# Kernel optimization log

Hardware: AMD Instinct MI355X
Metric: run time of the kernel (lower is better)

The kernel has to match this reference:

```python
import jax, jax.numpy as jnp
import numpy as np
import math

B, T, C, H = 2, 2048, 1024, 16
D = C // H  # head dim = 64

def setup_inputs() -> dict:
    key = jax.random.key(0)
    ks = jax.random.split(key, 5)
    scale_in = 1.0 / math.sqrt(C)
    x = jax.random.normal(ks[0], (B, T, C), dtype=jnp.float32)
    W_attn = jax.random.normal(ks[1], (C, 3 * C), dtype=jnp.float32) * scale_in
    b_attn = jnp.zeros((3 * C,), dtype=jnp.float32)
    W_proj = jax.random.normal(ks[2], (C, C), dtype=jnp.float32) * scale_in
    b_proj = jnp.zeros((C,), dtype=jnp.float32)
    return {"x": x, "W_attn": W_attn, "b_attn": b_attn, "W_proj": W_proj, "b_proj": b_proj}

def reference(x, W_attn, b_attn, W_proj, b_proj):
    qkv = x @ W_attn + b_attn                      # [B,T,3C]
    q, k, v = jnp.split(qkv, 3, axis=2)            # each [B,T,C]
    def heads(t):
        return t.reshape(B, T, H, D).transpose(0, 2, 1, 3)  # [B,H,T,D]
    q, k, v = heads(q), heads(k), heads(v)
    # NOTE: original scales by 1/sqrt(n_embd), not 1/sqrt(head_dim)
    scores = jnp.einsum('bhtd,bhsd->bhts', q, k) / math.sqrt(C)  # [B,H,T,T]
    mask = jnp.tril(jnp.ones((T, T), dtype=scores.dtype))
    scores = scores + (mask - 1.0) * 1e9
    attn = jax.nn.softmax(scores, axis=-1)
    out = jnp.einsum('bhts,bhsd->bhtd', attn, v)   # [B,H,T,D]
    out = out.transpose(0, 2, 1, 3).reshape(B, T, C)
    return out @ W_proj + b_proj
```

## Files before the change

kernel.cpp:

```cpp
#include <hip/hip_runtime.h>
#include <hip/hip_bf16.h>


typedef __attribute__((ext_vector_type(8))) short bf16x8;
typedef __attribute__((ext_vector_type(4))) short bf16x4;
typedef __attribute__((ext_vector_type(4))) float f32x4;

__device__ __forceinline__ short f2bs(float f) {
    union { __hip_bfloat16 h; short s; } u;
    u.h = __float2bfloat16(f);
    return u.s;
}

__device__ __forceinline__ short f2bs_trunc(float f) {
    return (short)(__float_as_uint(f) >> 16);
}

#define GLOAD_LDS16(gp, lp)                                                        \
    __builtin_amdgcn_global_load_lds((const __attribute__((address_space(1))) void*)(gp), \
                                     (__attribute__((address_space(3))) void*)(lp), 16, 0, 0)

__global__ __launch_bounds__(256) void convx(
    const float* __restrict__ X, short* __restrict__ Xb)
{
    const size_t i = ((size_t)blockIdx.x * 256 + threadIdx.x) * 8;
    float4 a = *(const float4*)(X + i);
    float4 b = *(const float4*)(X + i + 4);
    bf16x8 s;
    s[0] = f2bs(a.x); s[1] = f2bs(a.y); s[2] = f2bs(a.z); s[3] = f2bs(a.w);
    s[4] = f2bs(b.x); s[5] = f2bs(b.y); s[6] = f2bs(b.z); s[7] = f2bs(b.w);
    *(bf16x8*)(Xb + i) = s;
}

__global__ __launch_bounds__(256) void convt(
    const float* __restrict__ W, short* __restrict__ Wt, int K, int N)
{
    __shared__ short t[64 * 72];
    const int tid = threadIdx.x;
    const int n0 = blockIdx.x * 64, k0 = blockIdx.y * 64;
    #pragma unroll
    for (int i = 0; i < 4; i++) {
        int k = (tid >> 4) + i * 16;
        int n = (tid & 15) * 4;
        float4 v = *(const float4*)(W + (size_t)(k0 + k) * N + n0 + n);
        t[(n + 0) * 72 + k] = f2bs(v.x);
        t[(n + 1) * 72 + k] = f2bs(v.y);
        t[(n + 2) * 72 + k] = f2bs(v.z);
        t[(n + 3) * 72 + k] = f2bs(v.w);
    }
    __syncthreads();
    #pragma unroll
    for (int i = 0; i < 2; i++) {
        int n  = (tid >> 3) + i * 32;
        int kc = (tid & 7) * 8;
        bf16x8 v = *(const bf16x8*)&t[n * 72 + kc];
        *(bf16x8*)(Wt + (size_t)(n0 + n) * K + k0 + kc) = v;
    }
}

__global__ __launch_bounds__(512) void qkv_gemm(
    const short* __restrict__ Xb, const short* __restrict__ Wt,
    const float* __restrict__ bias,
    short* __restrict__ Qw, short* __restrict__ Kw, short* __restrict__ Vt)
{
    __shared__ short LB[57344];

    const int tid  = threadIdx.x;
    const int lane = tid & 63;
    const int wid  = tid >> 6;
    const int wm = wid >> 2, wn = wid & 3;
    const int g = lane >> 4, cc = lane & 15;
    const int sw = cc & 7;

    const int bid  = blockIdx.x;
    const int wgid = (bid & 7) * 32 + (bid >> 3);
    const int n0 = (wgid >> 4) * 192;
    const int m0 = (wgid & 15) * 256;

    f32x4 acc[8][3];
    const f32x4 z4 = {0.f, 0.f, 0.f, 0.f};
    #pragma unroll
    for (int i = 0; i < 8; i++)
        #pragma unroll
        for (int j = 0; j < 3; j++) acc[i][j] = z4;

    auto STAGE = [&](int t, int buf) {
        const int k0 = t * 64;
        short* Ab = LB + buf * 16384;
        short* Bb = LB + 32768 + buf * 12288;
        #pragma unroll
        for (int j = 0; j < 4; j++) {
            int c = j * 512 + wid * 64 + lane;
            int row = c >> 3, sch = (c & 7) ^ (row & 7);
            GLOAD_LDS16(Xb + (size_t)(m0 + row) * 1024 + k0 + sch * 8, Ab + c * 8);
        }
        #pragma unroll
        for (int j = 0; j < 3; j++) {
            int c = j * 512 + wid * 64 + lane;
            int row = c >> 3, sch = (c & 7) ^ (row & 7);
            GLOAD_LDS16(Wt + (size_t)(n0 + row) * 1024 + k0 + sch * 8, Bb + c * 8);
        }
    };

    STAGE(0, 0);
    STAGE(1, 1);
    asm volatile("s_waitcnt vmcnt(7)" ::: "memory");
    asm volatile("s_barrier" ::: "memory");

    const int NT = 16;
    for (int t = 0; t < NT; t++) {
        const short* Ab = LB + (t & 1) * 16384;
        const short* Bb = LB + 32768 + (t & 1) * 12288;

        bf16x8 bfr[3][2];
        #pragma unroll
        for (int nf = 0; nf < 3; nf++)
            #pragma unroll
            for (int kk = 0; kk < 2; kk++)
                bfr[nf][kk] = *(const bf16x8*)&Bb[(wn * 48 + nf * 16 + cc) * 64 +
                                                  ((kk * 4 + g) ^ sw) * 8];
        {
            bf16x8 af[4][2];
            #pragma unroll
            for (int mf = 0; mf < 4; mf++)
                #pragma unroll
                for (int kk = 0; kk < 2; kk++)
                    af[mf][kk] = *(const bf16x8*)&Ab[(wm * 128 + mf * 16 + cc) * 64 +
                                                     ((kk * 4 + g) ^ sw) * 8];
            __builtin_amdgcn_s_setprio(1);
            #pragma unroll
            for (int mf = 0; mf < 4; mf++)
                #pragma unroll
                for (int nf = 0; nf < 3; nf++)
                    #pragma unroll
                    for (int kk = 0; kk < 2; kk++)
                        acc[mf][nf] = __builtin_amdgcn_mfma_f32_16x16x32_bf16(
                            af[mf][kk], bfr[nf][kk], acc[mf][nf], 0, 0, 0);
            __builtin_amdgcn_s_setprio(0);
        }
        {
            bf16x8 af[4][2];
            #pragma unroll
            for (int mf = 0; mf < 4; mf++)
                #pragma unroll
                for (int kk = 0; kk < 2; kk++)
                    af[mf][kk] = *(const bf16x8*)&Ab[(wm * 128 + (mf + 4) * 16 + cc) * 64 +
                                                     ((kk * 4 + g) ^ sw) * 8];
            __builtin_amdgcn_s_setprio(1);
            #pragma unroll
            for (int mf = 0; mf < 4; mf++)
                #pragma unroll
                for (int nf = 0; nf < 3; nf++)
                    #pragma unroll
                    for (int kk = 0; kk < 2; kk++)
                        acc[mf + 4][nf] = __builtin_amdgcn_mfma_f32_16x16x32_bf16(
                            af[mf][kk], bfr[nf][kk], acc[mf + 4][nf], 0, 0, 0);
            __builtin_amdgcn_s_setprio(0);
        }

        asm volatile("s_barrier" ::: "memory");
        if (t + 2 < NT) {
            STAGE(t + 2, t & 1);
            asm volatile("s_waitcnt vmcnt(7)" ::: "memory");
            asm volatile("s_barrier" ::: "memory");
        } else if (t + 1 < NT) {
            asm volatile("s_waitcnt vmcnt(0)" ::: "memory");
            asm volatile("s_barrier" ::: "memory");
        }
    }

    const float QSCALE = 0.04508422976f;
    const int vs = (n0 > 2048) ? n0 : 2048;
    const int nV = n0 + 192 - vs;
    short* Vstage = LB;

    __syncthreads();

    #pragma unroll
    for (int nf = 0; nf < 3; nf++) {
        int col = n0 + wn * 48 + nf * 16 + cc;
        int which = col >> 10;
        int ci = col & 1023;
        int h = ci >> 6, d = ci & 63;
        float bv = bias[col];
        #pragma unroll
        for (int mf = 0; mf < 8; mf++) {
            if (which == 2) {
                int tl = wm * 128 + mf * 16 + g * 4;
                int pl = (tl & ~31) | (((tl >> 2) & 3) * 8 + ((tl >> 4) & 1) * 4);
                bf16x4 pk;
                #pragma unroll
                for (int r = 0; r < 4; r++) pk[r] = f2bs(acc[mf][nf][r] + bv);
                *(bf16x4*)&Vstage[(col - vs) * 264 + pl] = pk;
            } else {
                #pragma unroll
                for (int r = 0; r < 4; r++) {
                    int row = m0 + wm * 128 + mf * 16 + g * 4 + r;
                    int b = row >> 11, tt = row & 2047;
                    int bh = b * 16 + h;
                    float v = acc[mf][nf][r] + bv;
                    if (which == 0) Qw[((size_t)bh * 2048 + tt) * 64 + d] = f2bs(v * QSCALE);
                    else            Kw[((size_t)bh * 2048 + tt) * 64 + d] = f2bs(v);
                }
            }
        }
    }

    if (nV > 0) {
        __syncthreads();
        const int bb = m0 >> 11;
        const int tbase = m0 & 2047;
        const int total = nV * 32;
        for (int cidx = tid; cidx < total; cidx += 512) {
            int vc = cidx >> 5, toff = (cidx & 31) * 8;
            bf16x8 v = *(const bf16x8*)&Vstage[vc * 264 + toff];
            int col = vs + vc;
            int ci = col & 1023;
            int h2 = ci >> 6, d2 = ci & 63;
            *(bf16x8*)(Vt + ((size_t)(bb * 16 + h2) * 64 + d2) * 2048 + tbase + toff) = v;
        }
    }
}

__global__ __launch_bounds__(256) void attn_v13(
    const short* __restrict__ Qw, const short* __restrict__ Kw,
    const short* __restrict__ Vt, short* __restrict__ Aout)
{
    __shared__ short Klds[2][64 * 64];
    __shared__ short Vlds[2][64 * 64];
    const int tid  = threadIdx.x;
    const int lane = tid & 63;
    const int wid  = tid >> 6;
    const int g = lane >> 4, cc = lane & 15;
    const int bid = blockIdx.x;
    const int bh = bid & 31;
    const int g4 = bid >> 5;
    const int b = bh >> 4, h = bh & 15;
    const short* Qb = Qw + (size_t)bh * 2048 * 64;
    const short* Kb = Kw + (size_t)bh * 2048 * 64;
    const short* Vb = Vt + (size_t)bh * 64 * 2048;

    const f32x4 z4 = {0.f, 0.f, 0.f, 0.f};

    auto STAGE = [&](int t, int buf) {
        const int kv0 = t * 64;
        #pragma unroll
        for (int j = 0; j < 2; j++) {
            int c = tid + j * 256;
            int row = c >> 3, sch = (c & 7) ^ (row & 7);
            GLOAD_LDS16(Kb + (size_t)(kv0 + row) * 64 + sch * 8, &Klds[buf][c * 8]);
            GLOAD_LDS16(Vb + (size_t)row * 2048 + kv0 + sch * 8, &Vlds[buf][c * 8]);
        }
    };

    #pragma unroll
    for (int phase = 0; phase < 2; phase++) {
        const int grp = phase ? g4 : (31 - g4);
        const int q0 = grp * 64 + wid * 16;
        const int NT = grp + 1;

        bf16x8 qf0[2];
        #pragma unroll
        for (int ds = 0; ds < 2; ds++)
            qf0[ds] = *(const bf16x8*)(Qb + (q0 + cc) * 64 + ds * 32 + g * 8);

        f32x4 o[4];
        #pragma unroll
        for (int ch = 0; ch < 4; ch++) o[ch] = z4;
        float m_r = -1e30f, l_l = 0.f;

        STAGE(0, 0);
        STAGE(1, 1);
        asm volatile("s_waitcnt vmcnt(4)" ::: "memory");
        asm volatile("s_barrier" ::: "memory");

        for (int t = 0; t < NT; t++) {
            const int kv0 = t * 64;
            const short* Kt = Klds[t & 1];
            const short* Vt_ = Vlds[t & 1];
            const bool masked = (t == NT - 1);

            bf16x8 kf[8];
            #pragma unroll
            for (int kvc = 0; kvc < 4; kvc++) {
                int row = kvc * 16 + cc;
                #pragma unroll
                for (int ds = 0; ds < 2; ds++)
                    kf[kvc * 2 + ds] = *(const bf16x8*)&Kt[row * 64 +
                                                           (((ds * 4 + g) ^ (row & 7)) * 8)];
            }
            f32x4 s_[4];
            #pragma unroll
            for (int kvc = 0; kvc < 4; kvc++) {
                s_[kvc] = z4;
                #pragma unroll
                for (int ds = 0; ds < 2; ds++)
                    s_[kvc] = __builtin_amdgcn_mfma_f32_16x16x32_bf16(
                        kf[kvc * 2 + ds], qf0[ds], s_[kvc], 0, 0, 0);
            }
            bf16x8 vf[8];
            #pragma unroll
            for (int kvh = 0; kvh < 2; kvh++)
                #pragma unroll
                for (int ch = 0; ch < 4; ch++) {
                    int row = ch * 16 + cc;
                    vf[kvh * 4 + ch] = *(const bf16x8*)&Vt_[row * 64 +
                                                            (((kvh * 4 + g) ^ (row & 7)) * 8)];
                }

            bf16x8 pb_[2];
            {
                float sv[16];
                #pragma unroll
                for (int kvc = 0; kvc < 4; kvc++)
                    #pragma unroll
                    for (int r = 0; r < 4; r++) {
                        float v = s_[kvc][r];
                        if (masked) {
                            int kv = kv0 + kvc * 16 + g * 4 + r;
                            v = (kv <= q0 + cc) ? v : -1e30f;
                        }
                        sv[kvc * 4 + r] = v;
                    }
                float lm = sv[0];
                #pragma unroll
                for (int i = 1; i < 16; i++) lm = fmaxf(lm, sv[i]);
                if (__any(lm > m_r + 6.0f)) {
                    float mx = fmaxf(lm, __shfl_xor(lm, 16));
                    mx = fmaxf(mx, __shfl_xor(mx, 32));
                    float mn = fmaxf(m_r, mx);
                    float a = exp2f(m_r - mn);
                    #pragma unroll
                    for (int ch = 0; ch < 4; ch++)
                        #pragma unroll
                        for (int r = 0; r < 4; r++) o[ch][r] *= a;
                    l_l *= a;
                    m_r = mn;
                }
                float rs = 0.f;
                #pragma unroll
                for (int i = 0; i < 16; i++) {
                    float p = exp2f(sv[i] - m_r);
                    pb_[i >> 3][i & 7] = f2bs_trunc(p);
                    rs += p;
                }
                l_l += rs;
            }
            #pragma unroll
            for (int kvh = 0; kvh < 2; kvh++)
                #pragma unroll
                for (int ch = 0; ch < 4; ch++)
                    o[ch] = __builtin_amdgcn_mfma_f32_16x16x32_bf16(
                        vf[kvh * 4 + ch], pb_[kvh], o[ch], 0, 0, 0);

            asm volatile("s_barrier" ::: "memory");
            if (t + 2 < NT) {
                STAGE(t + 2, t & 1);
                asm volatile("s_waitcnt vmcnt(4)" ::: "memory");
                asm volatile("s_barrier" ::: "memory");
            } else if (t + 1 < NT) {
                asm volatile("s_waitcnt vmcnt(0)" ::: "memory");
                asm volatile("s_barrier" ::: "memory");
            }
        }

        float lt = l_l;
        lt += __shfl_xor(lt, 16);
        lt += __shfl_xor(lt, 32);
        float rl = 1.0f / lt;
        const int t2 = q0 + cc;
        #pragma unroll
        for (int ch = 0; ch < 4; ch++) {
            bf16x4 ov;
            #pragma unroll
            for (int r = 0; r < 4; r++) ov[r] = f2bs(o[ch][r] * rl);
            *(bf16x4*)(Aout + ((size_t)b * 2048 + t2) * 1024 + h * 64 + ch * 16 + g * 4) = ov;
        }
        __syncthreads();
    }
}

__global__ __launch_bounds__(512) void proj_gemm(
    const short* __restrict__ A, const short* __restrict__ Wt,
    const float* __restrict__ bias, float* __restrict__ Out)
{
    __shared__ short Alds[2][256 * 64];
    __shared__ short Blds[2][64 * 64];
    const int tid  = threadIdx.x;
    const int lane = tid & 63;
    const int wid  = tid >> 6;
    const int wm = wid >> 1, wn = wid & 1;
    const int g = lane >> 4, cc = lane & 15;
    const int sw = cc & 7;

    const int bid  = blockIdx.x;
    const int wgid = (bid & 7) * 32 + (bid >> 3);
    const int n0 = (wgid >> 4) * 64;
    const int m0 = (wgid & 15) * 256;

    f32x4 acc[4][2];
    const f32x4 z4 = {0.f, 0.f, 0.f, 0.f};
    #pragma unroll
    for (int i = 0; i < 4; i++)
        #pragma unroll
        for (int j = 0; j < 2; j++) acc[i][j] = z4;

    auto STAGE = [&](int t, int buf) {
        const int k0 = t * 64;
        #pragma unroll
        for (int j = 0; j < 4; j++) {
            int c = j * 512 + wid * 64 + lane;
            int row = c >> 3, sch = (c & 7) ^ (row & 7);
            GLOAD_LDS16(A + (size_t)(m0 + row) * 1024 + k0 + sch * 8,
                        &Alds[buf][c * 8]);
        }
        {
            int c = wid * 64 + lane;
            int row = c >> 3, sch = (c & 7) ^ (row & 7);
            GLOAD_LDS16(Wt + (size_t)(n0 + row) * 1024 + k0 + sch * 8,
                        &Blds[buf][c * 8]);
        }
    };

    STAGE(0, 0);
    STAGE(1, 1);
    asm volatile("s_waitcnt vmcnt(5)" ::: "memory");
    asm volatile("s_barrier" ::: "memory");

    const int NT = 16;
    for (int t = 0; t < NT; t++) {
        const short* Ab = Alds[t & 1];
        const short* Bb = Blds[t & 1];

        bf16x8 bfr[2][2];
        #pragma unroll
        for (int nf = 0; nf < 2; nf++)
            #pragma unroll
            for (int kk = 0; kk < 2; kk++)
                bfr[nf][kk] = *(const bf16x8*)&Bb[(wn * 32 + nf * 16 + cc) * 64 +
                                                  ((kk * 4 + g) ^ sw) * 8];
        bf16x8 af[4][2];
        #pragma unroll
        for (int mf = 0; mf < 4; mf++)
            #pragma unroll
            for (int kk = 0; kk < 2; kk++)
                af[mf][kk] = *(const bf16x8*)&Ab[(wm * 64 + mf * 16 + cc) * 64 +
                                                 ((kk * 4 + g) ^ sw) * 8];
        __builtin_amdgcn_s_setprio(1);
        #pragma unroll
        for (int mf = 0; mf < 4; mf++)
            #pragma unroll
            for (int nf = 0; nf < 2; nf++)
                #pragma unroll
                for (int kk = 0; kk < 2; kk++)
                    acc[mf][nf] = __builtin_amdgcn_mfma_f32_16x16x32_bf16(
                        af[mf][kk], bfr[nf][kk], acc[mf][nf], 0, 0, 0);
        __builtin_amdgcn_s_setprio(0);

        asm volatile("s_barrier" ::: "memory");
        if (t + 2 < NT) {
            STAGE(t + 2, t & 1);
            asm volatile("s_waitcnt vmcnt(5)" ::: "memory");
            asm volatile("s_barrier" ::: "memory");
        } else if (t + 1 < NT) {
            asm volatile("s_waitcnt vmcnt(0)" ::: "memory");
            asm volatile("s_barrier" ::: "memory");
        }
    }

    #pragma unroll
    for (int nf = 0; nf < 2; nf++) {
        int col = n0 + wn * 32 + nf * 16 + cc;
        float bv = bias[col];
        #pragma unroll
        for (int mf = 0; mf < 4; mf++) {
            #pragma unroll
            for (int r = 0; r < 4; r++) {
                int row = m0 + wm * 64 + mf * 16 + g * 4 + r;
                Out[(size_t)row * 1024 + col] = acc[mf][nf][r] + bv;
            }
        }
    }
}

extern "C" void kernel_launch(void* const* d_in, const int* in_sizes, int n_in,
                              void* d_out, int out_size, void* d_ws, size_t ws_size,
                              hipStream_t stream)
{
    const float* x      = (const float*)d_in[0];
    const float* W_attn = (const float*)d_in[1];
    const float* b_attn = (const float*)d_in[2];
    const float* W_proj = (const float*)d_in[3];
    const float* b_proj = (const float*)d_in[4];
    float* out = (float*)d_out;

    const size_t SZ = (size_t)4096 * 1024;
    short* R1 = (short*)d_ws;
    short* Qw = R1 + SZ;
    short* Kw = Qw + SZ;
    short* Vt = Kw + SZ;

    short* Wt_attn = R1;
    short* Aout    = R1;
    short* Wt_proj = Qw;
    short* Xb      = (short*)d_out;

    convx<<<dim3(2048), 256, 0, stream>>>(x, Xb);
    convt<<<dim3(48, 16), 256, 0, stream>>>(W_attn, Wt_attn, 1024, 3072);
    qkv_gemm<<<dim3(256), 512, 0, stream>>>(Xb, Wt_attn, b_attn, Qw, Kw, Vt);
    attn_v13<<<dim3(512), 256, 0, stream>>>(Qw, Kw, Vt, Aout);
    convt<<<dim3(16, 16), 256, 0, stream>>>(W_proj, Wt_proj, 1024, 1024);
    proj_gemm<<<dim3(256), 512, 0, stream>>>(Aout, Wt_proj, b_proj, out);
}
```

Before: 111.5 us.

## Halve tile sizes in QKV GEMM and attention to double workgroup counts

The QKV GEMM now uses 128-row M tiles instead of 256, with 512 workgroups and a smaller LDS footprint and accumulator set. The attention kernel uses 2-wave workgroups covering 32 query rows each, launched as 1024 blocks, and keeps causal pairing of early and late groups to balance load. A tree max reduction replaces the serial one. The goal is better occupancy and CU fill on the 256-CU device, at the cost of more redundant K/V and weight loads per output and less reuse per tile.

Result: slower. 118.0 us (+5.8%).

```diff
diff --git a/kernel.cpp b/kernel.cpp
--- a/kernel.cpp
+++ b/kernel.cpp
@@ -63,7 +63,7 @@
     const float* __restrict__ bias,
     short* __restrict__ Qw, short* __restrict__ Kw, short* __restrict__ Vt)
 {
-    __shared__ short LB[57344];
+    __shared__ short LB[40960];
 
     const int tid  = threadIdx.x;
     const int lane = tid & 63;
@@ -73,30 +73,30 @@
     const int sw = cc & 7;
 
     const int bid  = blockIdx.x;
-    const int wgid = (bid & 7) * 32 + (bid >> 3);
-    const int n0 = (wgid >> 4) * 192;
-    const int m0 = (wgid & 15) * 256;
-
-    f32x4 acc[8][3];
+    const int wgid = (bid & 7) * 64 + (bid >> 3);
+    const int n0 = (wgid >> 5) * 192;
+    const int m0 = (wgid & 31) * 128;
+
+    f32x4 acc[4][3];
     const f32x4 z4 = {0.f, 0.f, 0.f, 0.f};
     #pragma unroll
-    for (int i = 0; i < 8; i++)
+    for (int i = 0; i < 4; i++)
         #pragma unroll
         for (int j = 0; j < 3; j++) acc[i][j] = z4;
 
     auto STAGE = [&](int t, int buf) {
         const int k0 = t * 64;
-        short* Ab = LB + buf * 16384;
-        short* Bb = LB + 32768 + buf * 12288;
-        #pragma unroll
-        for (int j = 0; j < 4; j++) {
-            int c = j * 512 + wid * 64 + lane;
+        short* Ab = LB + buf * 8192;
+        short* Bb = LB + 16384 + buf * 12288;
+        #pragma unroll
+        for (int j = 0; j < 2; j++) {
+            int c = j * 512 + tid;
             int row = c >> 3, sch = (c & 7) ^ (row & 7);
             GLOAD_LDS16(Xb + (size_t)(m0 + row) * 1024 + k0 + sch * 8, Ab + c * 8);
         }
         #pragma unroll
         for (int j = 0; j < 3; j++) {
-            int c = j * 512 + wid * 64 + lane;
+            int c = j * 512 + tid;
             int row = c >> 3, sch = (c & 7) ^ (row & 7);
             GLOAD_LDS16(Wt + (size_t)(n0 + row) * 1024 + k0 + sch * 8, Bb + c * 8);
         }
@@ -104,13 +104,13 @@
 
     STAGE(0, 0);
     STAGE(1, 1);
-    asm volatile("s_waitcnt vmcnt(7)" ::: "memory");
+    asm volatile("s_waitcnt vmcnt(5)" ::: "memory");
     asm volatile("s_barrier" ::: "memory");
 
     const int NT = 16;
     for (int t = 0; t < NT; t++) {
-        const short* Ab = LB + (t & 1) * 16384;
-        const short* Bb = LB + 32768 + (t & 1) * 12288;
+        const short* Ab = LB + (t & 1) * 8192;
+        const short* Bb = LB + 16384 + (t & 1) * 12288;
 
         bf16x8 bfr[3][2];
         #pragma unroll
@@ -119,49 +119,28 @@
             for (int kk = 0; kk < 2; kk++)
                 bfr[nf][kk] = *(const bf16x8*)&Bb[(wn * 48 + nf * 16 + cc) * 64 +
                                                   ((kk * 4 + g) ^ sw) * 8];
-        {
-            bf16x8 af[4][2];
-            #pragma unroll
-            for (int mf = 0; mf < 4; mf++)
+        bf16x8 af[4][2];
+        #pragma unroll
+        for (int mf = 0; mf < 4; mf++)
+            #pragma unroll
+            for (int kk = 0; kk < 2; kk++)
+                af[mf][kk] = *(const bf16x8*)&Ab[(wm * 64 + mf * 16 + cc) * 64 +
+                                                 ((kk * 4 + g) ^ sw) * 8];
+        __builtin_amdgcn_s_setprio(1);
+        #pragma unroll
+        for (int mf = 0; mf < 4; mf++)
+            #pragma unroll
+            for (int nf = 0; nf < 3; nf++)
                 #pragma unroll
                 for (int kk = 0; kk < 2; kk++)
-                    af[mf][kk] = *(const bf16x8*)&Ab[(wm * 128 + mf * 16 + cc) * 64 +
-                                                     ((kk * 4 + g) ^ sw) * 8];
-            __builtin_amdgcn_s_setprio(1);
-            #pragma unroll
-            for (int mf = 0; mf < 4; mf++)
-                #pragma unroll
-                for (int nf = 0; nf < 3; nf++)
-                    #pragma unroll
-                    for (int kk = 0; kk < 2; kk++)
-                        acc[mf][nf] = __builtin_amdgcn_mfma_f32_16x16x32_bf16(
-                            af[mf][kk], bfr[nf][kk], acc[mf][nf], 0, 0, 0);
-            __builtin_amdgcn_s_setprio(0);
-        }
-        {
-            bf16x8 af[4][2];
-            #pragma unroll
-            for (int mf = 0; mf < 4; mf++)
-                #pragma unroll
-                for (int kk = 0; kk < 2; kk++)
-                    af[mf][kk] = *(const bf16x8*)&Ab[(wm * 128 + (mf + 4) * 16 + cc) * 64 +
-                                                     ((kk * 4 + g) ^ sw) * 8];
-            __builtin_amdgcn_s_setprio(1);
-            #pragma unroll
-            for (int mf = 0; mf < 4; mf++)
-                #pragma unroll
-                for (int nf = 0; nf < 3; nf++)
-                    #pragma unroll
-                    for (int kk = 0; kk < 2; kk++)
-                        acc[mf + 4][nf] = __builtin_amdgcn_mfma_f32_16x16x32_bf16(
-                            af[mf][kk], bfr[nf][kk], acc[mf + 4][nf], 0, 0, 0);
-            __builtin_amdgcn_s_setprio(0);
-        }
+                    acc[mf][nf] = __builtin_amdgcn_mfma_f32_16x16x32_bf16(
+                        af[mf][kk], bfr[nf][kk], acc[mf][nf], 0, 0, 0);
+        __builtin_amdgcn_s_setprio(0);
 
         asm volatile("s_barrier" ::: "memory");
         if (t + 2 < NT) {
             STAGE(t + 2, t & 1);
-            asm volatile("s_waitcnt vmcnt(7)" ::: "memory");
+            asm volatile("s_waitcnt vmcnt(5)" ::: "memory");
             asm volatile("s_barrier" ::: "memory");
         } else if (t + 1 < NT) {
             asm volatile("s_waitcnt vmcnt(0)" ::: "memory");
@@ -184,18 +163,18 @@
         int h = ci >> 6, d = ci & 63;
         float bv = bias[col];
         #pragma unroll
-        for (int mf = 0; mf < 8; mf++) {
+        for (int mf = 0; mf < 4; mf++) {
             if (which == 2) {
-                int tl = wm * 128 + mf * 16 + g * 4;
+                int tl = wm * 64 + mf * 16 + g * 4;
                 int pl = (tl & ~31) | (((tl >> 2) & 3) * 8 + ((tl >> 4) & 1) * 4);
                 bf16x4 pk;
                 #pragma unroll
                 for (int r = 0; r < 4; r++) pk[r] = f2bs(acc[mf][nf][r] + bv);
-                *(bf16x4*)&Vstage[(col - vs) * 264 + pl] = pk;
+                *(bf16x4*)&Vstage[(col - vs) * 136 + pl] = pk;
             } else {
                 #pragma unroll
                 for (int r = 0; r < 4; r++) {
-                    int row = m0 + wm * 128 + mf * 16 + g * 4 + r;
+                    int row = m0 + wm * 64 + mf * 16 + g * 4 + r;
                     int b = row >> 11, tt = row & 2047;
                     int bh = b * 16 + h;
                     float v = acc[mf][nf][r] + bv;
@@ -210,10 +189,10 @@
         __syncthreads();
         const int bb = m0 >> 11;
         const int tbase = m0 & 2047;
-        const int total = nV * 32;
+        const int total = nV * 16;
         for (int cidx = tid; cidx < total; cidx += 512) {
-            int vc = cidx >> 5, toff = (cidx & 31) * 8;
-            bf16x8 v = *(const bf16x8*)&Vstage[vc * 264 + toff];
+            int vc = cidx >> 4, toff = (cidx & 15) * 8;
+            bf16x8 v = *(const bf16x8*)&Vstage[vc * 136 + toff];
             int col = vs + vc;
             int ci = col & 1023;
             int h2 = ci >> 6, d2 = ci & 63;
@@ -222,7 +201,7 @@
     }
 }
 
-__global__ __launch_bounds__(256) void attn_v13(
+__global__ __launch_bounds__(128) void attn_v14(
     const short* __restrict__ Qw, const short* __restrict__ Kw,
     const short* __restrict__ Vt, short* __restrict__ Aout)
 {
@@ -234,7 +213,7 @@
     const int g = lane >> 4, cc = lane & 15;
     const int bid = blockIdx.x;
     const int bh = bid & 31;
-    const int g4 = bid >> 5;
+    const int j  = bid >> 5;
     const int b = bh >> 4, h = bh & 15;
     const short* Qb = Qw + (size_t)bh * 2048 * 64;
     const short* Kb = Kw + (size_t)bh * 2048 * 64;
@@ -245,8 +224,8 @@
     auto STAGE = [&](int t, int buf) {
         const int kv0 = t * 64;
         #pragma unroll
-        for (int j = 0; j < 2; j++) {
-            int c = tid + j * 256;
+        for (int jj = 0; jj < 4; jj++) {
+            int c = tid + jj * 128;
             int row = c >> 3, sch = (c & 7) ^ (row & 7);
             GLOAD_LDS16(Kb + (size_t)(kv0 + row) * 64 + sch * 8, &Klds[buf][c * 8]);
             GLOAD_LDS16(Vb + (size_t)row * 2048 + kv0 + sch * 8, &Vlds[buf][c * 8]);
@@ -255,9 +234,9 @@
 
     #pragma unroll
     for (int phase = 0; phase < 2; phase++) {
-        const int grp = phase ? g4 : (31 - g4);
-        const int q0 = grp * 64 + wid * 16;
-        const int NT = grp + 1;
+        const int grp = phase ? j : (63 - j);
+        const int q0 = grp * 32 + wid * 16;
+        const int NT = (grp >> 1) + 1;
 
         bf16x8 qf0[2];
         #pragma unroll
@@ -270,8 +249,8 @@
         float m_r = -1e30f, l_l = 0.f;
 
         STAGE(0, 0);
-        STAGE(1, 1);
-        asm volatile("s_waitcnt vmcnt(4)" ::: "memory");
+        if (NT > 1) STAGE(1, 1);
+        asm volatile("s_waitcnt vmcnt(8)" ::: "memory");
         asm volatile("s_barrier" ::: "memory");
 
         for (int t = 0; t < NT; t++) {
@@ -322,9 +301,12 @@
                         }
                         sv[kvc * 4 + r] = v;
                     }
-                float lm = sv[0];
-                #pragma unroll
-                for (int i = 1; i < 16; i++) lm = fmaxf(lm, sv[i]);
+                float m01 = fmaxf(sv[0], sv[1]),  m23 = fmaxf(sv[2], sv[3]);
+                float m45 = fmaxf(sv[4], sv[5]),  m67 = fmaxf(sv[6], sv[7]);
+                float m89 = fmaxf(sv[8], sv[9]),  mab = fmaxf(sv[10], sv[11]);
+                float mcd = fmaxf(sv[12], sv[13]), mef = fmaxf(sv[14], sv[15]);
+                float lm = fmaxf(fmaxf(fmaxf(m01, m23), fmaxf(m45, m67)),
+                                 fmaxf(fmaxf(m89, mab), fmaxf(mcd, mef)));
                 if (__any(lm > m_r + 6.0f)) {
                     float mx = fmaxf(lm, __shfl_xor(lm, 16));
                     mx = fmaxf(mx, __shfl_xor(mx, 32));
@@ -356,7 +338,7 @@
             asm volatile("s_barrier" ::: "memory");
             if (t + 2 < NT) {
                 STAGE(t + 2, t & 1);
-                asm volatile("s_waitcnt vmcnt(4)" ::: "memory");
+                asm volatile("s_waitcnt vmcnt(8)" ::: "memory");
                 asm volatile("s_barrier" ::: "memory");
             } else if (t + 1 < NT) {
                 asm volatile("s_waitcnt vmcnt(0)" ::: "memory");
@@ -507,8 +489,8 @@
 
     convx<<<dim3(2048), 256, 0, stream>>>(x, Xb);
     convt<<<dim3(48, 16), 256, 0, stream>>>(W_attn, Wt_attn, 1024, 3072);
-    qkv_gemm<<<dim3(256), 512, 0, stream>>>(Xb, Wt_attn, b_attn, Qw, Kw, Vt);
-    attn_v13<<<dim3(512), 256, 0, stream>>>(Qw, Kw, Vt, Aout);
+    qkv_gemm<<<dim3(512), 512, 0, stream>>>(Xb, Wt_attn, b_attn, Qw, Kw, Vt);
+    attn_v14<<<dim3(1024), 128, 0, stream>>>(Qw, Kw, Vt, Aout);
     convt<<<dim3(16, 16), 256, 0, stream>>>(W_proj, Wt_proj, 1024, 1024);
     proj_gemm<<<dim3(256), 512, 0, stream>>>(Aout, Wt_proj, b_proj, out);
 }
```
